# Performance work log

Measured on AMD Instinct MI355X. Metric: run time of the kernel, lower is better.

## Reference

```python
import jax, jax.numpy as jnp
import numpy as np

T = 4096   # total packed tokens
NQ = 16    # query heads
NK = 4     # kv heads (GQA)
HN = 128   # head dim


def setup_inputs() -> dict:
    key = jax.random.key(0)
    kq, kk, kv = jax.random.split(key, 3)
    return {
        "query": jax.random.normal(kq, (T, NQ, HN), dtype=jnp.float32),
        "key": jax.random.normal(kk, (T, NK, HN), dtype=jnp.float32),
        "value": jax.random.normal(kv, (T, NK, HN), dtype=jnp.float32),
        # packed varlen boundaries (4 sequences)
        "cu_seqlens": jnp.array([0, 1536, 2048, 3584, 4096], dtype=jnp.int32),
    }


def reference(query, key, value, cu_seqlens):
    t, nq, hn = query.shape
    nk = key.shape[1]
    rep = nq // nk  # GQA expansion factor
    scale = hn ** -0.5
    # [h, t, d] layout (matches torch unsqueeze(0).permute(0,2,1,3), batch=1)
    q = jnp.transpose(query, (1, 0, 2))
    k = jnp.repeat(jnp.transpose(key, (1, 0, 2)), rep, axis=0)
    v = jnp.repeat(jnp.transpose(value, (1, 0, 2)), rep, axis=0)
    # full scores [h, t, t]
    scores = jnp.einsum('hqd,hkd->hqk', q, k) * scale
    # block-diagonal causal mask from cu_seqlens
    idx = jnp.arange(t)
    seg = jnp.searchsorted(cu_seqlens[1:], idx, side='right')  # segment id per token
    allowed = (seg[:, None] == seg[None, :]) & (idx[None, :] <= idx[:, None])
    scores = jnp.where(allowed[None, :, :], scores, -jnp.inf)
    p = jax.nn.softmax(scores, axis=-1)  # every row keeps its diagonal -> no NaN
    out = jnp.einsum('hqk,hkd->hqd', p, v)
    # [t, nq*hn]
    return jnp.transpose(out, (1, 0, 2)).reshape(t, nq * hn)
```

## Files before the change

kernel.cpp:

```cpp
#include <hip/hip_runtime.h>
#include <hip/hip_bf16.h>
#include <cstdint>
#include <cstddef>

#define NQH 16
#define NKH 4
#define HN 128
#define QBLK 64
#define KBLK 32
#define QSCALE 0.12751589542585458f

typedef __bf16 bf16x8 __attribute__((ext_vector_type(8)));
typedef float f32x4 __attribute__((ext_vector_type(4)));

__device__ __forceinline__ void gload16(const void* g, void* l) {
  __builtin_amdgcn_global_load_lds(
      (const __attribute__((address_space(1))) void*)g,
      (__attribute__((address_space(3))) void*)l, 16, 0, 0);
}

__global__ __launch_bounds__(256) void cvt_kv(const float* __restrict__ K,
                                              const float* __restrict__ V,
                                              __bf16* __restrict__ Kb,
                                              __bf16* __restrict__ Vb, int T) {
  const int nkblk = T * NKH * HN / 8 / 256;
  const int bid = blockIdx.x;
  if (bid < nkblk) {
    const size_t idx8 = ((size_t)bid * 256 + threadIdx.x) * 8;
    const int d = (int)(idx8 & 127);
    const int kvh = (int)((idx8 >> 7) & 3);
    const size_t t = idx8 >> 9;
    float4 a = *(const float4*)&K[idx8];
    float4 b = *(const float4*)&K[idx8 + 4];
    bf16x8 f;
    f[0] = (__bf16)a.x; f[1] = (__bf16)a.y; f[2] = (__bf16)a.z; f[3] = (__bf16)a.w;
    f[4] = (__bf16)b.x; f[5] = (__bf16)b.y; f[6] = (__bf16)b.z; f[7] = (__bf16)b.w;
    *(bf16x8*)&Kb[(size_t)kvh * T * HN + t * HN + d] = f;
  } else {
    const int ob = (bid - nkblk) * 2 + (threadIdx.x >> 7);
    const int bx = ob & (T / 8 - 1);
    const int kvh = ob / (T / 8);
    const int d = threadIdx.x & 127;
    const int t0 = bx * 8;
    bf16x8 f;
#pragma unroll
    for (int i = 0; i < 8; ++i)
      f[i] = (__bf16)V[(size_t)(t0 + i) * (NKH * HN) + kvh * HN + d];
    *(bf16x8*)&Vb[(size_t)kvh * HN * T + (size_t)d * T + t0] = f;
  }
}

template <bool MASKED>
__device__ __forceinline__ void attn_iter(
    const char* Kc, const char* Vc, const bf16x8 qfA[4], const bf16x8 qfB[4],
    int ln, int hi, int vslot, int limA, float& mA, float& lA, f32x4* accA,
    float& mB, float& lB, f32x4* accB) {
  bf16x8 kf[2][4];
#pragma unroll
  for (int c = 0; c < 2; ++c)
#pragma unroll
    for (int kc = 0; kc < 4; ++kc)
      kf[c][kc] = *(const bf16x8*)(Kc + (c * 16 + ln) * 256 +
                                   (((kc * 4 + hi) ^ (ln & 7)) << 4));

  f32x4 sA[2], sB[2];
#pragma unroll
  for (int c = 0; c < 2; ++c) {
    sA[c] = (f32x4){0.f, 0.f, 0.f, 0.f};
    sB[c] = (f32x4){0.f, 0.f, 0.f, 0.f};
  }
  __builtin_amdgcn_s_setprio(1);
#pragma unroll
  for (int kc = 0; kc < 4; ++kc) {
#pragma unroll
    for (int c = 0; c < 2; ++c) {
      sA[c] = __builtin_amdgcn_mfma_f32_16x16x32_bf16(kf[c][kc], qfA[kc], sA[c], 0, 0, 0);
      sB[c] = __builtin_amdgcn_mfma_f32_16x16x32_bf16(kf[c][kc], qfB[kc], sB[c], 0, 0, 0);
    }
  }
  __builtin_amdgcn_s_setprio(0);

  if (MASKED) {
    const int limB = limA + 16;
#pragma unroll
    for (int c = 0; c < 2; ++c)
#pragma unroll
      for (int i = 0; i < 4; ++i) {
        const int koff = hi * 8 + c * 4 + i;
        sA[c][i] = (koff <= limA) ? sA[c][i] : -1e30f;
        sB[c][i] = (koff <= limB) ? sB[c][i] : -1e30f;
      }
  }

  const float lmA = fmaxf(fmaxf(fmaxf(sA[0][0], sA[0][1]), fmaxf(sA[0][2], sA[0][3])),
                          fmaxf(fmaxf(sA[1][0], sA[1][1]), fmaxf(sA[1][2], sA[1][3])));
  const float lmB = fmaxf(fmaxf(fmaxf(sB[0][0], sB[0][1]), fmaxf(sB[0][2], sB[0][3])),
                          fmaxf(fmaxf(sB[1][0], sB[1][1]), fmaxf(sB[1][2], sB[1][3])));
  if (__any((lmA > mA + 8.0f) | (lmB > mB + 8.0f))) {
    float mmA = fmaxf(lmA, __shfl_xor(lmA, 16));
    mmA = fmaxf(mmA, __shfl_xor(mmA, 32));
    float mmB = fmaxf(lmB, __shfl_xor(lmB, 16));
    mmB = fmaxf(mmB, __shfl_xor(mmB, 32));
    const float mnA = fmaxf(mA, mmA), mnB = fmaxf(mB, mmB);
    const float cA = exp2f(mA - mnA), cB = exp2f(mB - mnB);
    mA = mnA; mB = mnB;
    lA *= cA; lB *= cB;
#pragma unroll
    for (int dt = 0; dt < 8; ++dt) { accA[dt] *= cA; accB[dt] *= cB; }
  }

  float pA[2][4], pB[2][4];
  float psA = 0.f, psB = 0.f;
#pragma unroll
  for (int c = 0; c < 2; ++c)
#pragma unroll
    for (int i = 0; i < 4; ++i) {
      pA[c][i] = exp2f(sA[c][i] - mA); psA += pA[c][i];
      pB[c][i] = exp2f(sB[c][i] - mB); psB += pB[c][i];
    }
  lA += psA; lB += psB;

  bf16x8 paA, paB;
#pragma unroll
  for (int e = 0; e < 8; ++e) {
    paA[e] = (__bf16)pA[e >> 2][e & 3];
    paB[e] = (__bf16)pB[e >> 2][e & 3];
  }

  __builtin_amdgcn_s_setprio(1);
#pragma unroll
  for (int dt = 0; dt < 8; ++dt) {
    const bf16x8 vb = *(const bf16x8*)(Vc + (dt * 16 + ln) * 64 + vslot);
    accA[dt] = __builtin_amdgcn_mfma_f32_16x16x32_bf16(vb, paA, accA[dt], 0, 0, 0);
    accB[dt] = __builtin_amdgcn_mfma_f32_16x16x32_bf16(vb, paB, accB[dt], 0, 0, 0);
  }
  __builtin_amdgcn_s_setprio(0);
}

__global__ __launch_bounds__(256, 2) void attn_pipe(
    const float* __restrict__ Q, const __bf16* __restrict__ Kb,
    const __bf16* __restrict__ Vb, const int* __restrict__ cu,
    float* __restrict__ O, int T, int nseg) {
  const int tid = threadIdx.x;
  const int w = tid >> 6, lane = tid & 63;
  const int g = w >> 1, wv = w & 1;
  const int ln = lane & 15, hi = lane >> 4;

  const int bid = blockIdx.x;
  const int round = bid >> 8, pos = bid & 255;
  const int rr = (round & 1) ? ((round << 8) | (255 - pos)) : bid;
  const int h = rr & 15;
  const int my_rank = rr >> 4;
  const int kvh = h >> 2;

  __shared__ __align__(16) char smem[66064];
  float* ml1 = (float*)(smem + 65536);
  int* s_tile = (int*)(smem + 66048);

  if (w == 0) {
    const int t2 = lane;
    const int r0t = t2 << 6;
    int st = 0;
    for (int s = 1; s < nseg; ++s) { const int c = cu[s]; if (c <= r0t) st = c; }
    const int dep = r0t + QBLK - st;
    int rk = 0;
    for (int j = 0; j < 64; ++j) {
      const int dj = __shfl(dep, j);
      rk += (dj > dep) || (dj == dep && j < t2);
    }
    if (rk == my_rank) *s_tile = t2;
  }
  __syncthreads();
  const int r0 = *s_tile << 6;

  int st0 = 0;
  for (int s = 1; s < nseg; ++s) { const int c = cu[s]; if (c <= r0) st0 = c; }
  const int kstart = st0;
  const int n0 = (r0 + QBLK - kstart) >> 6;
  const int gbeg = kstart + g * n0 * KBLK;

  const __bf16* KbH = Kb + (size_t)kvh * T * HN;
  const __bf16* VbH = Vb + (size_t)kvh * HN * T;

  bf16x8 qfA[4], qfB[4];
  {
    const float* qpA = &Q[(size_t)(r0 + wv * 32 + ln) * (NQH * HN) + h * HN];
    const float* qpB = qpA + (size_t)16 * (NQH * HN);
#pragma unroll
    for (int kc = 0; kc < 4; ++kc) {
      float4 a0 = *(const float4*)(qpA + kc * 32 + hi * 8);
      float4 a1 = *(const float4*)(qpA + kc * 32 + hi * 8 + 4);
      float4 b0 = *(const float4*)(qpB + kc * 32 + hi * 8);
      float4 b1 = *(const float4*)(qpB + kc * 32 + hi * 8 + 4);
      bf16x8 fa, fb;
      fa[0] = (__bf16)(a0.x * QSCALE); fa[1] = (__bf16)(a0.y * QSCALE);
      fa[2] = (__bf16)(a0.z * QSCALE); fa[3] = (__bf16)(a0.w * QSCALE);
      fa[4] = (__bf16)(a1.x * QSCALE); fa[5] = (__bf16)(a1.y * QSCALE);
      fa[6] = (__bf16)(a1.z * QSCALE); fa[7] = (__bf16)(a1.w * QSCALE);
      fb[0] = (__bf16)(b0.x * QSCALE); fb[1] = (__bf16)(b0.y * QSCALE);
      fb[2] = (__bf16)(b0.z * QSCALE); fb[3] = (__bf16)(b0.w * QSCALE);
      fb[4] = (__bf16)(b1.x * QSCALE); fb[5] = (__bf16)(b1.y * QSCALE);
      fb[6] = (__bf16)(b1.z * QSCALE); fb[7] = (__bf16)(b1.w * QSCALE);
      qfA[kc] = fa; qfB[kc] = fb;
    }
  }

  float mA = 0.f, lA = 0.f, mB = 0.f, lB = 0.f;
  f32x4 accA[8], accB[8];
#pragma unroll
  for (int dt = 0; dt < 8; ++dt) {
    accA[dt] = (f32x4){0.f, 0.f, 0.f, 0.f};
    accB[dt] = (f32x4){0.f, 0.f, 0.f, 0.f};
  }

  const int gl = wv * 64 + lane;
  const int Rb = gl >> 4, sK = gl & 15;
  int key_j[4];
#pragma unroll
  for (int j = 0; j < 4; ++j)
    key_j[j] = ((Rb >> 2) << 3) + (Rb & 3) + ((j & 1) << 4) + ((j >> 1) << 2);
  const int kcolE = (sK ^ Rb) << 3;
  const int db = gl >> 2, sV = gl & 3;
  const int swz_d = (db & 3) ^ ((db >> 2) & 3);
  const int vkeyE = (sV ^ swz_d) << 3;
  const int vslot = ((hi ^ (ln & 3) ^ ((ln >> 2) & 3)) << 4);
  const int relA = wv * 32 + ln;

#define ISSUE_TILE(b, kb_)                                                     \
  {                                                                            \
    char* base_ = smem + (((g << 1) | (b)) << 14);                             \
    char* lK_ = base_ + gl * 16;                                               \
    char* lV_ = base_ + 8192 + gl * 16;                                        \
    _Pragma("unroll")                                                          \
    for (int j = 0; j < 4; ++j)                                                \
      gload16(KbH + (size_t)((kb_) + key_j[j]) * HN + kcolE, lK_ + j * 2048);  \
    _Pragma("unroll")                                                          \
    for (int j = 0; j < 4; ++j)                                                \
      gload16(VbH + (size_t)(db + 32 * j) * T + (kb_) + vkeyE, lV_ + j * 2048);\
  }

  ISSUE_TILE(0, gbeg);
  if (n0 > 1) ISSUE_TILE(1, gbeg + KBLK);

  for (int it = 0; it < n0; ++it) {
    const int cur = it & 1;
    if (it < n0 - 1) {
      asm volatile("s_waitcnt vmcnt(8)" ::: "memory");
    } else {
      asm volatile("s_waitcnt vmcnt(0)" ::: "memory");
    }
    __builtin_amdgcn_sched_barrier(0);
    __builtin_amdgcn_s_barrier();
    const char* tb = smem + (((g << 1) | cur) << 14);
    const int kb = gbeg + it * KBLK;
    if (kb >= r0)
      attn_iter<true>(tb, tb + 8192, qfA, qfB, ln, hi, vslot,
                      relA - (kb - r0), mA, lA, accA, mB, lB, accB);
    else
      attn_iter<false>(tb, tb + 8192, qfA, qfB, ln, hi, vslot, 0, mA, lA,
                       accA, mB, lB, accB);
    asm volatile("s_waitcnt lgkmcnt(0)" ::: "memory");
    __builtin_amdgcn_sched_barrier(0);
    __builtin_amdgcn_s_barrier();
    if (it + 2 < n0) ISSUE_TILE(cur, kb + 2 * KBLK);
  }
#undef ISSUE_TILE

  lA += __shfl_xor(lA, 16); lA += __shfl_xor(lA, 32);
  lB += __shfl_xor(lB, 16); lB += __shfl_xor(lB, 32);

  __syncthreads();

  float* accf = (float*)smem;
  if (g == 1) {
    if (hi == 0) {
      ml1[relA * 2] = mA;            ml1[relA * 2 + 1] = lA;
      ml1[(relA + 16) * 2] = mB;     ml1[(relA + 16) * 2 + 1] = lB;
    }
#pragma unroll
    for (int dt = 0; dt < 8; ++dt) {
      *(f32x4*)&accf[relA * 128 + ((dt ^ (relA & 7)) << 4) + (hi << 2)] = accA[dt];
      *(f32x4*)&accf[(relA + 16) * 128 + ((dt ^ ((relA + 16) & 7)) << 4) + (hi << 2)] = accB[dt];
    }
  }
  __syncthreads();
  if (g == 0) {
#pragma unroll
    for (int set = 0; set < 2; ++set) {
      const int row = relA + set * 16;
      const float mg = set ? mB : mA;
      const float lg = set ? lB : lA;
      f32x4* acc = set ? accB : accA;
      const float m1 = ml1[row * 2], l1v = ml1[row * 2 + 1];
      float c0 = 1.f, c1 = 0.f, l = lg;
      if (l1v != 0.f) {
        const float m = fmaxf(mg, m1);
        c0 = exp2f(mg - m); c1 = exp2f(m1 - m);
        l = lg * c0 + l1v * c1;
      }
      const float inv = 1.0f / l;
      float* op = &O[(size_t)(r0 + row) * (NQH * HN) + h * HN];
#pragma unroll
      for (int dt = 0; dt < 8; ++dt) {
        const f32x4 a1 = *(const f32x4*)&accf[row * 128 + ((dt ^ (row & 7)) << 4) + (hi << 2)];
        const f32x4 res = (acc[dt] * c0 + a1 * c1) * inv;
        *(f32x4*)&op[dt * 16 + hi * 4] = res;
      }
    }
  }
}

extern "C" void kernel_launch(void* const* d_in, const int* in_sizes, int n_in,
                              void* d_out, int out_size, void* d_ws, size_t ws_size,
                              hipStream_t stream) {
  const float* Q = (const float*)d_in[0];
  const float* K = (const float*)d_in[1];
  const float* V = (const float*)d_in[2];
  const int* cu = (const int*)d_in[3];
  float* O = (float*)d_out;

  const int T = in_sizes[0] / (NQH * HN);
  const int nseg = in_sizes[3] - 1;

  const size_t need = (size_t)2 * NKH * T * HN * sizeof(__bf16);
  if (ws_size < need) return;

  __bf16* Kb = (__bf16*)d_ws;
  __bf16* Vb = (__bf16*)d_ws + (size_t)NKH * T * HN;

  const int nkblk = T * NKH * HN / 8 / 256;
  cvt_kv<<<2 * nkblk, 256, 0, stream>>>(K, V, Kb, Vb, T);

  attn_pipe<<<1024, 256, 0, stream>>>(Q, Kb, Vb, cu, O, T, nseg);
}
```

Baseline: 65.19 us.

## Share KV tiles across all four query heads of a GQA group per block

Replaces the 256-thread per-head attention kernel with a 1024-thread kernel. Each block covers one KV head and a 64-row query tile for all four query heads that share it, so each K/V tile is loaded into LDS once and reused four times, cutting global and L2 traffic. The longest-first tile scheduling is dropped in favour of a simple block index mapping, and the cross-group merge is split into two passes so it fits in shared memory. The trade-offs are load imbalance with one large block per CU, a tighter register budget under the new launch bounds, and possible spills.

```diff
diff --git a/kernel.cpp b/kernel.cpp
--- a/kernel.cpp
+++ b/kernel.cpp
@@ -137,46 +137,30 @@
   __builtin_amdgcn_s_setprio(0);
 }
 
-__global__ __launch_bounds__(256, 2) void attn_pipe(
+__global__ __launch_bounds__(1024, 4) void attn_gqa(
     const float* __restrict__ Q, const __bf16* __restrict__ Kb,
     const __bf16* __restrict__ Vb, const int* __restrict__ cu,
     float* __restrict__ O, int T, int nseg) {
   const int tid = threadIdx.x;
   const int w = tid >> 6, lane = tid & 63;
-  const int g = w >> 1, wv = w & 1;
+  const int g = w >> 3;
+  const int sub = w & 7;
+  const int qh = sub >> 1, half = sub & 1;
   const int ln = lane & 15, hi = lane >> 4;
 
   const int bid = blockIdx.x;
-  const int round = bid >> 8, pos = bid & 255;
-  const int rr = (round & 1) ? ((round << 8) | (255 - pos)) : bid;
-  const int h = rr & 15;
-  const int my_rank = rr >> 4;
-  const int kvh = h >> 2;
-
-  __shared__ __align__(16) char smem[66064];
+  const int kvh = bid & 3;
+  const int r0 = (bid >> 2) << 6;
+  const int h = kvh * 4 + qh;
+
+  __shared__ __align__(16) char smem[67584];
   float* ml1 = (float*)(smem + 65536);
-  int* s_tile = (int*)(smem + 66048);
-
-  if (w == 0) {
-    const int t2 = lane;
-    const int r0t = t2 << 6;
-    int st = 0;
-    for (int s = 1; s < nseg; ++s) { const int c = cu[s]; if (c <= r0t) st = c; }
-    const int dep = r0t + QBLK - st;
-    int rk = 0;
-    for (int j = 0; j < 64; ++j) {
-      const int dj = __shfl(dep, j);
-      rk += (dj > dep) || (dj == dep && j < t2);
-    }
-    if (rk == my_rank) *s_tile = t2;
-  }
-  __syncthreads();
-  const int r0 = *s_tile << 6;
 
   int st0 = 0;
   for (int s = 1; s < nseg; ++s) { const int c = cu[s]; if (c <= r0) st0 = c; }
   const int kstart = st0;
-  const int n0 = (r0 + QBLK - kstart) >> 6;
+  const int nkb32 = (r0 + QBLK - kstart) >> 5;
+  const int n0 = nkb32 >> 1;
   const int gbeg = kstart + g * n0 * KBLK;
 
   const __bf16* KbH = Kb + (size_t)kvh * T * HN;
@@ -184,7 +168,7 @@
 
   bf16x8 qfA[4], qfB[4];
   {
-    const float* qpA = &Q[(size_t)(r0 + wv * 32 + ln) * (NQH * HN) + h * HN];
+    const float* qpA = &Q[(size_t)(r0 + half * 32 + ln) * (NQH * HN) + h * HN];
     const float* qpB = qpA + (size_t)16 * (NQH * HN);
 #pragma unroll
     for (int kc = 0; kc < 4; ++kc) {
@@ -213,30 +197,21 @@
     accB[dt] = (f32x4){0.f, 0.f, 0.f, 0.f};
   }
 
-  const int gl = wv * 64 + lane;
-  const int Rb = gl >> 4, sK = gl & 15;
-  int key_j[4];
-#pragma unroll
-  for (int j = 0; j < 4; ++j)
-    key_j[j] = ((Rb >> 2) << 3) + (Rb & 3) + ((j & 1) << 4) + ((j >> 1) << 2);
-  const int kcolE = (sK ^ Rb) << 3;
-  const int db = gl >> 2, sV = gl & 3;
-  const int swz_d = (db & 3) ^ ((db >> 2) & 3);
-  const int vkeyE = (sV ^ swz_d) << 3;
+  const int gl = (w & 7) * 64 + lane;
+  const int R = gl >> 4, sK = gl & 15;
+  const int keyoff = (((R & 15) >> 2) << 3) + ((R >> 4) << 2) + (R & 3);
+  const int kcolE = ((sK ^ (R & 7)) << 3);
+  const int d = gl >> 2, sV = gl & 3;
+  const int swz_d = (d & 3) ^ ((d >> 2) & 3);
+  const int vkeyE = ((sV ^ swz_d) << 3);
   const int vslot = ((hi ^ (ln & 3) ^ ((ln >> 2) & 3)) << 4);
-  const int relA = wv * 32 + ln;
+  const int relA = half * 32 + ln;
 
 #define ISSUE_TILE(b, kb_)                                                     \
   {                                                                            \
     char* base_ = smem + (((g << 1) | (b)) << 14);                             \
-    char* lK_ = base_ + gl * 16;                                               \
-    char* lV_ = base_ + 8192 + gl * 16;                                        \
-    _Pragma("unroll")                                                          \
-    for (int j = 0; j < 4; ++j)                                                \
-      gload16(KbH + (size_t)((kb_) + key_j[j]) * HN + kcolE, lK_ + j * 2048);  \
-    _Pragma("unroll")                                                          \
-    for (int j = 0; j < 4; ++j)                                                \
-      gload16(VbH + (size_t)(db + 32 * j) * T + (kb_) + vkeyE, lV_ + j * 2048);\
+    gload16(KbH + (size_t)((kb_) + keyoff) * HN + kcolE, base_ + gl * 16);     \
+    gload16(VbH + (size_t)d * T + (kb_) + vkeyE, base_ + 8192 + gl * 16);      \
   }
 
   ISSUE_TILE(0, gbeg);
@@ -245,7 +220,7 @@
   for (int it = 0; it < n0; ++it) {
     const int cur = it & 1;
     if (it < n0 - 1) {
-      asm volatile("s_waitcnt vmcnt(8)" ::: "memory");
+      asm volatile("s_waitcnt vmcnt(2)" ::: "memory");
     } else {
       asm volatile("s_waitcnt vmcnt(0)" ::: "memory");
     }
@@ -271,42 +246,47 @@
 
   __syncthreads();
 
-  float* accf = (float*)smem;
-  if (g == 1) {
-    if (hi == 0) {
-      ml1[relA * 2] = mA;            ml1[relA * 2 + 1] = lA;
-      ml1[(relA + 16) * 2] = mB;     ml1[(relA + 16) * 2 + 1] = lB;
-    }
-#pragma unroll
-    for (int dt = 0; dt < 8; ++dt) {
-      *(f32x4*)&accf[relA * 128 + ((dt ^ (relA & 7)) << 4) + (hi << 2)] = accA[dt];
-      *(f32x4*)&accf[(relA + 16) * 128 + ((dt ^ ((relA + 16) & 7)) << 4) + (hi << 2)] = accB[dt];
-    }
-  }
-  __syncthreads();
-  if (g == 0) {
-#pragma unroll
-    for (int set = 0; set < 2; ++set) {
-      const int row = relA + set * 16;
-      const float mg = set ? mB : mA;
-      const float lg = set ? lB : lA;
-      f32x4* acc = set ? accB : accA;
-      const float m1 = ml1[row * 2], l1v = ml1[row * 2 + 1];
-      float c0 = 1.f, c1 = 0.f, l = lg;
-      if (l1v != 0.f) {
-        const float m = fmaxf(mg, m1);
-        c0 = exp2f(mg - m); c1 = exp2f(m1 - m);
-        l = lg * c0 + l1v * c1;
+  if (g == 1 && hi == 0) {
+    ml1[(qh * 64 + relA) * 2] = mA;      ml1[(qh * 64 + relA) * 2 + 1] = lA;
+    ml1[(qh * 64 + relA + 16) * 2] = mB; ml1[(qh * 64 + relA + 16) * 2 + 1] = lB;
+  }
+#pragma unroll
+  for (int pass = 0; pass < 2; ++pass) {
+    float* accf = (float*)smem + (qh & 1) * 8192;
+    if (g == 1 && (qh >> 1) == pass) {
+#pragma unroll
+      for (int dt = 0; dt < 8; ++dt) {
+        *(f32x4*)&accf[relA * 128 + ((dt ^ (relA & 7)) << 4) + (hi << 2)] = accA[dt];
+        *(f32x4*)&accf[(relA + 16) * 128 + ((dt ^ ((relA + 16) & 7)) << 4) + (hi << 2)] = accB[dt];
       }
-      const float inv = 1.0f / l;
-      float* op = &O[(size_t)(r0 + row) * (NQH * HN) + h * HN];
-#pragma unroll
-      for (int dt = 0; dt < 8; ++dt) {
-        const f32x4 a1 = *(const f32x4*)&accf[row * 128 + ((dt ^ (row & 7)) << 4) + (hi << 2)];
-        const f32x4 res = (acc[dt] * c0 + a1 * c1) * inv;
-        *(f32x4*)&op[dt * 16 + hi * 4] = res;
+    }
+    __syncthreads();
+    if (g == 0 && (qh >> 1) == pass) {
+#pragma unroll
+      for (int set = 0; set < 2; ++set) {
+        const int row = relA + set * 16;
+        const float mg = set ? mB : mA;
+        const float lg = set ? lB : lA;
+        f32x4* acc = set ? accB : accA;
+        const float m1 = ml1[(qh * 64 + row) * 2];
+        const float l1v = ml1[(qh * 64 + row) * 2 + 1];
+        float c0 = 1.f, c1 = 0.f, l = lg;
+        if (l1v != 0.f) {
+          const float m = fmaxf(mg, m1);
+          c0 = exp2f(mg - m); c1 = exp2f(m1 - m);
+          l = lg * c0 + l1v * c1;
+        }
+        const float inv = 1.0f / l;
+        float* op = &O[(size_t)(r0 + row) * (NQH * HN) + h * HN];
+#pragma unroll
+        for (int dt = 0; dt < 8; ++dt) {
+          const f32x4 a1 = *(const f32x4*)&accf[row * 128 + ((dt ^ (row & 7)) << 4) + (hi << 2)];
+          const f32x4 res = (acc[dt] * c0 + a1 * c1) * inv;
+          *(f32x4*)&op[dt * 16 + hi * 4] = res;
+        }
       }
     }
+    __syncthreads();
   }
 }
 
@@ -331,5 +311,5 @@
   const int nkblk = T * NKH * HN / 8 / 256;
   cvt_kv<<<2 * nkblk, 256, 0, stream>>>(K, V, Kb, Vb, T);
 
-  attn_pipe<<<1024, 256, 0, stream>>>(Q, Kb, Vb, cu, O, T, nseg);
-}
+  attn_gqa<<<(T / QBLK) * NKH, 1024, 0, stream>>>(Q, Kb, Vb, cu, O, T, nseg);
+}
```

Measured after the change: 211.3 us. 3.24x slower.

## Share K/V LDS tiles across two GQA query heads per workgroup

Applied to the files above, without the earlier changes.

Each workgroup now runs 512 threads covering two query heads that map to the same KV head, so each K/V tile loaded into LDS serves both heads. Per-thread load counts and the vmcnt wait threshold are halved, and the final merge buffers are split per head. This targets redundant K/V global loads and LDS fills across heads. The grid drops to half as many, larger blocks, which can reduce occupancy flexibility and tail balance.

```diff
diff --git a/kernel.cpp b/kernel.cpp
--- a/kernel.cpp
+++ b/kernel.cpp
@@ -137,25 +137,26 @@
   __builtin_amdgcn_s_setprio(0);
 }
 
-__global__ __launch_bounds__(256, 2) void attn_pipe(
+__global__ __launch_bounds__(512, 2) void attn_gqa2(
     const float* __restrict__ Q, const __bf16* __restrict__ Kb,
     const __bf16* __restrict__ Vb, const int* __restrict__ cu,
     float* __restrict__ O, int T, int nseg) {
   const int tid = threadIdx.x;
   const int w = tid >> 6, lane = tid & 63;
-  const int g = w >> 1, wv = w & 1;
+  const int g = w >> 2;
+  const int hp = (w >> 1) & 1, half = w & 1;
   const int ln = lane & 15, hi = lane >> 4;
 
   const int bid = blockIdx.x;
-  const int round = bid >> 8, pos = bid & 255;
-  const int rr = (round & 1) ? ((round << 8) | (255 - pos)) : bid;
-  const int h = rr & 15;
-  const int my_rank = rr >> 4;
-  const int kvh = h >> 2;
-
-  __shared__ __align__(16) char smem[66064];
+  const int rr = (bid < 256) ? bid : (767 - bid);
+  const int tile_rank = rr >> 3;
+  const int y = rr & 7;
+  const int kvh = y >> 1;
+  const int h = kvh * 4 + (y & 1) * 2 + hp;
+
+  __shared__ __align__(16) char smem[66576];
   float* ml1 = (float*)(smem + 65536);
-  int* s_tile = (int*)(smem + 66048);
+  int* s_tile = (int*)(smem + 66560);
 
   if (w == 0) {
     const int t2 = lane;
@@ -168,7 +169,7 @@
       const int dj = __shfl(dep, j);
       rk += (dj > dep) || (dj == dep && j < t2);
     }
-    if (rk == my_rank) *s_tile = t2;
+    if (rk == tile_rank) *s_tile = t2;
   }
   __syncthreads();
   const int r0 = *s_tile << 6;
@@ -184,7 +185,7 @@
 
   bf16x8 qfA[4], qfB[4];
   {
-    const float* qpA = &Q[(size_t)(r0 + wv * 32 + ln) * (NQH * HN) + h * HN];
+    const float* qpA = &Q[(size_t)(r0 + half * 32 + ln) * (NQH * HN) + h * HN];
     const float* qpB = qpA + (size_t)16 * (NQH * HN);
 #pragma unroll
     for (int kc = 0; kc < 4; ++kc) {
@@ -213,30 +214,25 @@
     accB[dt] = (f32x4){0.f, 0.f, 0.f, 0.f};
   }
 
-  const int gl = wv * 64 + lane;
+  const int gl = ((w & 3) << 6) + lane;
   const int Rb = gl >> 4, sK = gl & 15;
-  int key_j[4];
-#pragma unroll
-  for (int j = 0; j < 4; ++j)
-    key_j[j] = ((Rb >> 2) << 3) + (Rb & 3) + ((j & 1) << 4) + ((j >> 1) << 2);
-  const int kcolE = (sK ^ Rb) << 3;
-  const int db = gl >> 2, sV = gl & 3;
-  const int swz_d = (db & 3) ^ ((db >> 2) & 3);
+  const int keyoff = ((Rb >> 2) << 3) + (Rb & 3);
+  const int kcolE = (sK ^ (Rb & 7)) << 3;
+  const int d = gl >> 2, sV = gl & 3;
+  const int swz_d = (d & 3) ^ ((d >> 2) & 3);
   const int vkeyE = (sV ^ swz_d) << 3;
   const int vslot = ((hi ^ (ln & 3) ^ ((ln >> 2) & 3)) << 4);
-  const int relA = wv * 32 + ln;
-
-#define ISSUE_TILE(b, kb_)                                                     \
-  {                                                                            \
-    char* base_ = smem + (((g << 1) | (b)) << 14);                             \
-    char* lK_ = base_ + gl * 16;                                               \
-    char* lV_ = base_ + 8192 + gl * 16;                                        \
-    _Pragma("unroll")                                                          \
-    for (int j = 0; j < 4; ++j)                                                \
-      gload16(KbH + (size_t)((kb_) + key_j[j]) * HN + kcolE, lK_ + j * 2048);  \
-    _Pragma("unroll")                                                          \
-    for (int j = 0; j < 4; ++j)                                                \
-      gload16(VbH + (size_t)(db + 32 * j) * T + (kb_) + vkeyE, lV_ + j * 2048);\
+  const int relA = half * 32 + ln;
+
+#define ISSUE_TILE(b, kb_)                                                      \
+  {                                                                             \
+    char* base_ = smem + (((g << 1) | (b)) << 14);                              \
+    gload16(KbH + (size_t)((kb_) + keyoff) * HN + kcolE, base_ + gl * 16);      \
+    gload16(KbH + (size_t)((kb_) + keyoff + 4) * HN + kcolE,                    \
+            base_ + gl * 16 + 4096);                                            \
+    gload16(VbH + (size_t)d * T + (kb_) + vkeyE, base_ + 8192 + gl * 16);       \
+    gload16(VbH + (size_t)(d + 64) * T + (kb_) + vkeyE,                         \
+            base_ + 8192 + gl * 16 + 4096);                                     \
   }
 
   ISSUE_TILE(0, gbeg);
@@ -245,7 +241,7 @@
   for (int it = 0; it < n0; ++it) {
     const int cur = it & 1;
     if (it < n0 - 1) {
-      asm volatile("s_waitcnt vmcnt(8)" ::: "memory");
+      asm volatile("s_waitcnt vmcnt(4)" ::: "memory");
     } else {
       asm volatile("s_waitcnt vmcnt(0)" ::: "memory");
     }
@@ -271,11 +267,11 @@
 
   __syncthreads();
 
-  float* accf = (float*)smem;
+  float* accf = (float*)smem + hp * 8192;
   if (g == 1) {
     if (hi == 0) {
-      ml1[relA * 2] = mA;            ml1[relA * 2 + 1] = lA;
-      ml1[(relA + 16) * 2] = mB;     ml1[(relA + 16) * 2 + 1] = lB;
+      ml1[(hp * 64 + relA) * 2] = mA;      ml1[(hp * 64 + relA) * 2 + 1] = lA;
+      ml1[(hp * 64 + relA + 16) * 2] = mB; ml1[(hp * 64 + relA + 16) * 2 + 1] = lB;
     }
 #pragma unroll
     for (int dt = 0; dt < 8; ++dt) {
@@ -291,7 +287,8 @@
       const float mg = set ? mB : mA;
       const float lg = set ? lB : lA;
       f32x4* acc = set ? accB : accA;
-      const float m1 = ml1[row * 2], l1v = ml1[row * 2 + 1];
+      const float m1 = ml1[(hp * 64 + row) * 2];
+      const float l1v = ml1[(hp * 64 + row) * 2 + 1];
       float c0 = 1.f, c1 = 0.f, l = lg;
       if (l1v != 0.f) {
         const float m = fmaxf(mg, m1);
@@ -331,5 +328,5 @@
   const int nkblk = T * NKH * HN / 8 / 256;
   cvt_kv<<<2 * nkblk, 256, 0, stream>>>(K, V, Kb, Vb, T);
 
-  attn_pipe<<<1024, 256, 0, stream>>>(Q, Kb, Vb, cu, O, T, nseg);
-}
+  attn_gqa2<<<512, 512, 0, stream>>>(Q, Kb, Vb, cu, O, T, nseg);
+}
```

Measured after the change: 76.34 us. +17.1%, slower.
